# Kernel optimization log

Measured on AMD Instinct MI355X. Metric: run time of the kernel, lower is better.

Reference implementation:

```python
import jax, jax.numpy as jnp
import numpy as np


def setup_inputs() -> dict:
    key = jax.random.key(0)
    k0, k1, k2, k3 = jax.random.split(key, 4)
    B, T, C = 4, 2048, 1024
    x = jax.random.normal(k0, (B, T, C), dtype=jnp.float32)
    s = C ** -0.5  # init-scale for weights so activations stay O(1)
    Wq = jax.random.normal(k1, (C, C), dtype=jnp.float32) * s
    Wk = jax.random.normal(k2, (C, C), dtype=jnp.float32) * s
    Wv = jax.random.normal(k3, (C, C), dtype=jnp.float32) * s
    return {"x": x, "Wq": Wq, "Wk": Wk, "Wv": Wv}


def reference(x, Wq, Wk, Wv):
    B, T, C = x.shape
    # torch nn.Linear: y = x @ W.T
    q = jnp.einsum('btc,dc->btd', x, Wq)
    k = jnp.einsum('btc,dc->btd', x, Wk)
    v = jnp.einsum('btc,dc->btd', x, Wv)
    scale = C ** -0.5
    wei = jnp.einsum('btd,bsd->bts', q, k) * scale  # [B, T, T]
    causal = jnp.tril(jnp.ones((T, T), dtype=bool))
    wei = jnp.where(causal, wei, -jnp.inf)
    wei = jax.nn.softmax(wei, axis=-1)
    out = jnp.einsum('bts,bsd->btd', wei, v)
    return out
```

## Files before the change

### kernel.cpp

```cpp
#include <hip/hip_runtime.h>
#include <hip/hip_bf16.h>
#include <math.h>

#define B_ 4
#define T_ 2048
#define C_ 1024
#define M_ (B_*T_)

typedef __attribute__((ext_vector_type(8))) __bf16 bf16x8;
typedef __attribute__((ext_vector_type(4))) float floatx4;

__device__ inline float bf2f(unsigned short u){
    return __uint_as_float(((unsigned)u) << 16);
}
__device__ inline unsigned short f2bf(float f){
    unsigned u = __float_as_uint(f);
    unsigned r = (u + 0x7fffu + ((u >> 16) & 1u)) >> 16;
    return (unsigned short)r;
}

__device__ inline void llds16(const unsigned short* g, unsigned short* lds){
    __builtin_amdgcn_global_load_lds(
        (const __attribute__((address_space(1))) unsigned int*)g,
        (__attribute__((address_space(3))) unsigned int*)(unsigned int)(uintptr_t)lds,
        16, 0, 0);
}

#define NX_ (M_*C_/4)
#define NW_ (C_*C_/4)
#define NL4_ (M_/4)
__global__ __launch_bounds__(256) void cast_all(
    const float* __restrict__ x, const float* __restrict__ wq,
    const float* __restrict__ wk, const float* __restrict__ wv,
    unsigned short* __restrict__ xb, unsigned short* __restrict__ wb,
    float* __restrict__ l)
{
    int i = blockIdx.x * 256 + threadIdx.x;
    const float* src; unsigned short* dst; int idx;
    if (i < NX_){ src = x; dst = xb; idx = i; }
    else if (i < NX_ + 3 * NW_){
        i -= NX_;
        int w = i / NW_; idx = i - w * NW_;
        src = (w == 0) ? wq : ((w == 1) ? wk : wv);
        dst = wb + (size_t)w * C_ * C_;
    } else {
        ((float4*)l)[i - NX_ - 3 * NW_] = make_float4(0.f, 0.f, 0.f, 0.f);
        return;
    }
    float4 v = ((const float4*)src)[idx];
    ((ushort4*)dst)[idx] = make_ushort4(f2bf(v.x), f2bf(v.y), f2bf(v.z), f2bf(v.w));
}

template<int WM, int WN>
__device__ inline void gemm_core(const unsigned short* __restrict__ A,
                                 const unsigned short* __restrict__ Bm,
                                 int lda, int ldb, int m0, int n0, int kTiles,
                                 unsigned short* As, unsigned short* Bs,
                                 floatx4 (*acc)[WN/16])
{
    const int tid  = threadIdx.x;
    const int lane = tid & 63;
    const int wave = tid >> 6;
    const int wm = (wave >> 1) * WM;
    const int wn = (wave & 1) * WN;
    const int fr = lane & 15;
    const int fq = lane >> 4;
    const int cxor = fr & 7;
    const int sr = lane >> 3;
    const int sc = ((lane & 7) ^ ((lane >> 3) & 7)) * 8;

    const unsigned short* gA = A  + (size_t)(m0 + wave * (WM/2) + sr) * lda + sc;
    const unsigned short* gB = Bm + (size_t)(n0 + wave * (WN/2) + sr) * ldb + sc;
    unsigned short* ldsA = As + wave * (WM/2) * 64;
    unsigned short* ldsB = Bs + wave * (WN/2) * 64;

    for (int kt = 0; kt < kTiles; kt++){
        const int k0 = kt * 64;
        __syncthreads();
        #pragma unroll
        for (int i = 0; i < WM/16; i++)
            llds16(gA + (size_t)(i * 8) * lda + k0, ldsA + i * 8 * 64);
        #pragma unroll
        for (int i = 0; i < WN/16; i++)
            llds16(gB + (size_t)(i * 8) * ldb + k0, ldsB + i * 8 * 64);
        __syncthreads();
        #pragma unroll
        for (int ks = 0; ks < 64; ks += 32){
            const int cpos = (((ks >> 3) + fq) ^ cxor) * 8;
            bf16x8 af[WM/16], bv[WN/16];
            #pragma unroll
            for (int i = 0; i < WM/16; i++)
                af[i] = *(const bf16x8*)(As + (wm + i*16 + fr) * 64 + cpos);
            #pragma unroll
            for (int j = 0; j < WN/16; j++)
                bv[j] = *(const bf16x8*)(Bs + (wn + j*16 + fr) * 64 + cpos);
            #pragma unroll
            for (int i = 0; i < WM/16; i++)
                #pragma unroll
                for (int j = 0; j < WN/16; j++)
                    acc[i][j] = __builtin_amdgcn_mfma_f32_16x16x32_bf16(af[i], bv[j], acc[i][j], 0, 0, 0);
        }
    }
}

template<int WM, int WN>
__device__ inline void gemm_core8(const unsigned short* __restrict__ A,
                                  const unsigned short* __restrict__ Bm,
                                  int lda, int ldb, int m0, int n0, int kTiles,
                                  unsigned short* As, unsigned short* Bs,
                                  floatx4 (*acc)[WN/16])
{
    const int tid  = threadIdx.x;
    const int lane = tid & 63;
    const int wave = tid >> 6;
    const int wm = (wave >> 1) * WM;
    const int wn = (wave & 1) * WN;
    const int fr = lane & 15;
    const int fq = lane >> 4;
    const int cxor = fr & 7;
    const int sr = lane >> 3;
    const int sc = ((lane & 7) ^ ((lane >> 3) & 7)) * 8;

    const unsigned short* gA = A  + (size_t)(m0 + wave * (WM/2) + sr) * lda + sc;
    const unsigned short* gB = Bm + (size_t)(n0 + wave * (WN/4) + sr) * ldb + sc;
    unsigned short* ldsA = As + wave * (WM/2) * 64;
    unsigned short* ldsB = Bs + wave * (WN/4) * 64;

    for (int kt = 0; kt < kTiles; kt++){
        const int k0 = kt * 64;
        __syncthreads();
        #pragma unroll
        for (int i = 0; i < WM/16; i++)
            llds16(gA + (size_t)(i * 8) * lda + k0, ldsA + i * 8 * 64);
        #pragma unroll
        for (int i = 0; i < WN/32; i++)
            llds16(gB + (size_t)(i * 8) * ldb + k0, ldsB + i * 8 * 64);
        __syncthreads();
        #pragma unroll
        for (int ks = 0; ks < 64; ks += 32){
            const int cpos = (((ks >> 3) + fq) ^ cxor) * 8;
            bf16x8 af[WM/16], bv[WN/16];
            #pragma unroll
            for (int i = 0; i < WM/16; i++)
                af[i] = *(const bf16x8*)(As + (wm + i*16 + fr) * 64 + cpos);
            #pragma unroll
            for (int j = 0; j < WN/16; j++)
                bv[j] = *(const bf16x8*)(Bs + (wn + j*16 + fr) * 64 + cpos);
            #pragma unroll
            for (int i = 0; i < WM/16; i++)
                #pragma unroll
                for (int j = 0; j < WN/16; j++)
                    acc[i][j] = __builtin_amdgcn_mfma_f32_16x16x32_bf16(af[i], bv[j], acc[i][j], 0, 0, 0);
        }
    }
}

__global__ __launch_bounds__(256, 4) void proj_gemm(
    const unsigned short* __restrict__ xb,
    const unsigned short* __restrict__ Wb,
    unsigned short* __restrict__ Qb, unsigned short* __restrict__ Kb,
    unsigned short* __restrict__ Vt)
{
    __shared__ unsigned short As[128 * 64];
    __shared__ unsigned short Bs[128 * 64];
    const int L = blockIdx.x;
    const int k = L & 7, j = L >> 3;
    const int m0 = (k * 8 + (j & 7)) * 128;
    const int n0 = ((j >> 3) & 7) * 128;
    const int z  = j >> 6;
    const unsigned short* W = Wb + (size_t)z * C_ * C_;

    floatx4 acc[4][4];
    #pragma unroll
    for (int i = 0; i < 4; i++)
        #pragma unroll
        for (int jj = 0; jj < 4; jj++) acc[i][jj] = (floatx4){0.f,0.f,0.f,0.f};
    gemm_core<64, 64>(xb, W, C_, C_, m0, n0, C_ / 64, As, Bs, acc);

    const int lane = threadIdx.x & 63, wave = threadIdx.x >> 6;
    const int wm = (wave >> 1) * 64, wn = (wave & 1) * 64;
    const int fr = lane & 15, fq = lane >> 4;

    if (z < 2){
        unsigned short* Y = z ? Kb : Qb;
        #pragma unroll
        for (int i = 0; i < 4; i++)
            #pragma unroll
            for (int jj = 0; jj < 4; jj++)
                #pragma unroll
                for (int r = 0; r < 4; r++){
                    int row = m0 + wm + i*16 + fq*4 + r;
                    int col = n0 + wn + jj*16 + fr;
                    Y[(size_t)row * C_ + col] = f2bf(acc[i][jj][r]);
                }
    } else {
        #pragma unroll
        for (int i = 0; i < 4; i++)
            #pragma unroll
            for (int jj = 0; jj < 4; jj++){
                int row = m0 + wm + i*16 + fq*4;
                int col = n0 + wn + jj*16 + fr;
                int b = row / T_, t = row % T_;
                ushort4 o = make_ushort4(f2bf(acc[i][jj][0]), f2bf(acc[i][jj][1]),
                                         f2bf(acc[i][jj][2]), f2bf(acc[i][jj][3]));
                *(ushort4*)&Vt[(size_t)b * C_ * T_ + (size_t)col * T_ + t] = o;
            }
    }
}

__global__ __launch_bounds__(512, 4) void score_gemm(
    const unsigned short* __restrict__ Qb, const unsigned short* __restrict__ Kb,
    unsigned short* __restrict__ P, float* __restrict__ l)
{
    const int L = blockIdx.x;
    const int xcd = L & 7, j = L >> 3;
    const int b  = xcd >> 1;
    const int p  = j / 17, rr = j % 17;
    const int kk = 2 * p + (xcd & 1);
    int ti, si;
    if (rr <= 15 - kk){ ti = 15 - kk; si = rr; }
    else              { ti = kk;      si = rr - (16 - kk); }
    const int t0 = ti * 128, s0 = si * 128;

    __shared__ unsigned short As[128 * 64];
    __shared__ unsigned short Bs[128 * 64];
    floatx4 acc[2][4];
    #pragma unroll
    for (int i = 0; i < 2; i++)
        #pragma unroll
        for (int jj = 0; jj < 4; jj++) acc[i][jj] = (floatx4){0.f,0.f,0.f,0.f};
    gemm_core8<32, 64>(Qb + (size_t)b * T_ * C_, Kb + (size_t)b * T_ * C_,
                       C_, C_, t0, s0, C_ / 64, As, Bs, acc);

    const int lane = threadIdx.x & 63, wave = threadIdx.x >> 6;
    const int wm = (wave >> 1) * 32, wn = (wave & 1) * 64;
    const int fr = lane & 15, fq = lane >> 4;
    unsigned short* Pb = P + (size_t)b * T_ * T_;
    const float scale = 0.03125f;
    float rsl[2][4];
    #pragma unroll
    for (int i = 0; i < 2; i++)
        #pragma unroll
        for (int r2 = 0; r2 < 4; r2++) rsl[i][r2] = 0.f;

    #pragma unroll
    for (int i = 0; i < 2; i++)
        #pragma unroll
        for (int jj = 0; jj < 4; jj++)
            #pragma unroll
            for (int r2 = 0; r2 < 4; r2++){
                int t = t0 + wm + i*16 + fq*4 + r2;
                int s = s0 + wn + jj*16 + fr;
                float v = (s <= t) ? __expf(acc[i][jj][r2] * scale) : 0.f;
                rsl[i][r2] += v;
                Pb[(size_t)t * T_ + s] = f2bf(v);
            }
    #pragma unroll
    for (int i = 0; i < 2; i++)
        #pragma unroll
        for (int r2 = 0; r2 < 4; r2++){
            float v = rsl[i][r2];
            v += __shfl_xor(v, 1, 64);
            v += __shfl_xor(v, 2, 64);
            v += __shfl_xor(v, 4, 64);
            v += __shfl_xor(v, 8, 64);
            if (fr == 0){
                int t = t0 + wm + i*16 + fq*4 + r2;
                atomicAdd(&l[(size_t)b * T_ + t], v);
            }
        }
}

__global__ __launch_bounds__(256, 4) void pv_gemm(
    const unsigned short* __restrict__ P, const unsigned short* __restrict__ Vt,
    const float* __restrict__ l, float* __restrict__ out)
{
    const int L = blockIdx.x;
    const int xcd = L & 7, j = L >> 3;
    const int b  = xcd >> 1;
    const int p  = j >> 4;
    const int n0 = (j & 15) * 64;
    const int kk = 2 * p + (xcd & 1);

    __shared__ unsigned short As[128 * 64];
    __shared__ unsigned short Bs[64 * 64];

    const int lane = threadIdx.x & 63, wave = threadIdx.x >> 6;
    const int wm = (wave >> 1) * 64, wn = (wave & 1) * 32;
    const int fr = lane & 15, fq = lane >> 4;
    float* ob = out + (size_t)b * T_ * C_;
    const float* lb = l + (size_t)b * T_;

    #pragma unroll
    for (int phase = 0; phase < 2; phase++){
        const int ti = phase ? kk : (15 - kk);
        const int t0 = ti * 128;
        const int kTiles = 2 * (ti + 1);

        floatx4 acc[4][2];
        #pragma unroll
        for (int i = 0; i < 4; i++)
            #pragma unroll
            for (int jj = 0; jj < 2; jj++) acc[i][jj] = (floatx4){0.f,0.f,0.f,0.f};
        gemm_core<64, 32>(P + (size_t)b * T_ * T_, Vt + (size_t)b * C_ * T_,
                          T_, T_, t0, n0, kTiles, As, Bs, acc);

        #pragma unroll
        for (int i = 0; i < 4; i++){
            float inv[4];
            #pragma unroll
            for (int r2 = 0; r2 < 4; r2++)
                inv[r2] = 1.f / lb[t0 + wm + i*16 + fq*4 + r2];
            #pragma unroll
            for (int jj = 0; jj < 2; jj++)
                #pragma unroll
                for (int r2 = 0; r2 < 4; r2++){
                    int t = t0 + wm + i*16 + fq*4 + r2;
                    int d = n0 + wn + jj*16 + fr;
                    ob[(size_t)t * C_ + d] = acc[i][jj][r2] * inv[r2];
                }
        }
    }
}

extern "C" void kernel_launch(void* const* d_in, const int* in_sizes, int n_in,
                              void* d_out, int out_size, void* d_ws, size_t ws_size,
                              hipStream_t stream)
{
    const float* x  = (const float*)d_in[0];
    const float* Wq = (const float*)d_in[1];
    const float* Wk = (const float*)d_in[2];
    const float* Wv = (const float*)d_in[3];
    float* out = (float*)d_out;

    unsigned short* Qb = (unsigned short*)d_ws;
    unsigned short* Kb = Qb + (size_t)M_ * C_;
    unsigned short* Vt = Kb + (size_t)M_ * C_;
    unsigned short* P  = Vt + (size_t)M_ * C_;
    float* l = (float*)(P + (size_t)M_ * T_);
    unsigned short* xb = P;
    unsigned short* Wb = P + (size_t)M_ * C_;

    cast_all<<<(NX_ + 3 * NW_ + NL4_ + 255) / 256, 256, 0, stream>>>(
        x, Wq, Wk, Wv, xb, Wb, l);
    proj_gemm <<<1536, 256, 0, stream>>>(xb, Wb, Qb, Kb, Vt);
    score_gemm<<<544, 512, 0, stream>>>(Qb, Kb, P, l);
    pv_gemm   <<<512, 256, 0, stream>>>(P, Vt, l, out);
}
```

Measured before the change: 203.4 us.

## Double-buffer LDS tiles with vmcnt-counted prefetch in score and PV GEMMs

Replaces the single-buffer load/sync/compute loop in the score and PV GEMM cores with double-buffered LDS. The next k-tile is issued via global_load_lds before the current one is computed, and explicit s_waitcnt vmcnt and barriers control the hazards. This is meant to hide global load latency behind MFMA work. It doubles LDS use per block, which may lower occupancy, and relies on hand-written waitcnt counts matching the issued loads.

```diff
diff --git a/kernel.cpp b/kernel.cpp
--- a/kernel.cpp
+++ b/kernel.cpp
@@ -25,6 +25,15 @@
         (__attribute__((address_space(3))) unsigned int*)(unsigned int)(uintptr_t)lds,
         16, 0, 0);
 }
+
+template<int N> __device__ inline void vmwait(){
+    static_assert(N==0 || N==4 || N==6 || N==8, "add literal");
+    if constexpr (N==0) asm volatile("s_waitcnt vmcnt(0)" ::: "memory");
+    else if constexpr (N==4) asm volatile("s_waitcnt vmcnt(4)" ::: "memory");
+    else if constexpr (N==6) asm volatile("s_waitcnt vmcnt(6)" ::: "memory");
+    else if constexpr (N==8) asm volatile("s_waitcnt vmcnt(8)" ::: "memory");
+}
+__device__ inline void lgkm0(){ asm volatile("s_waitcnt lgkmcnt(0)" ::: "memory"); }
 
 #define NX_ (M_*C_/4)
 #define NW_ (C_*C_/4)
@@ -104,12 +113,16 @@
 }
 
 template<int WM, int WN>
-__device__ inline void gemm_core8(const unsigned short* __restrict__ A,
-                                  const unsigned short* __restrict__ Bm,
-                                  int lda, int ldb, int m0, int n0, int kTiles,
-                                  unsigned short* As, unsigned short* Bs,
-                                  floatx4 (*acc)[WN/16])
-{
+__device__ inline void gemm_core_cnt(const unsigned short* __restrict__ A,
+                                     const unsigned short* __restrict__ Bm,
+                                     int lda, int ldb, int m0, int n0, int kTiles,
+                                     unsigned short* As, unsigned short* Bs,
+                                     floatx4 (*acc)[WN/16])
+{
+    const int NL  = WM/16 + WN/16;
+    const int ASZ = 2 * WM * 64;
+    const int BSZ = 2 * WN * 64;
+
     const int tid  = threadIdx.x;
     const int lane = tid & 63;
     const int wave = tid >> 6;
@@ -122,36 +135,132 @@
     const int sc = ((lane & 7) ^ ((lane >> 3) & 7)) * 8;
 
     const unsigned short* gA = A  + (size_t)(m0 + wave * (WM/2) + sr) * lda + sc;
+    const unsigned short* gB = Bm + (size_t)(n0 + wave * (WN/2) + sr) * ldb + sc;
+    unsigned short* ldsA = As + wave * (WM/2) * 64;
+    unsigned short* ldsB = Bs + wave * (WN/2) * 64;
+
+    __syncthreads();
+    #pragma unroll
+    for (int i = 0; i < WM/16; i++)
+        llds16(gA + (size_t)(i * 8) * lda, ldsA + i * 8 * 64);
+    #pragma unroll
+    for (int i = 0; i < WN/16; i++)
+        llds16(gB + (size_t)(i * 8) * ldb, ldsB + i * 8 * 64);
+
+    int cur = 0;
+    for (int kt = 0; kt < kTiles; kt++){
+        if (kt + 1 < kTiles){
+            const int nk0 = (kt + 1) * 64;
+            unsigned short* lA = ldsA + (cur ^ 1) * ASZ;
+            unsigned short* lB = ldsB + (cur ^ 1) * BSZ;
+            #pragma unroll
+            for (int i = 0; i < WM/16; i++)
+                llds16(gA + (size_t)(i * 8) * lda + nk0, lA + i * 8 * 64);
+            #pragma unroll
+            for (int i = 0; i < WN/16; i++)
+                llds16(gB + (size_t)(i * 8) * ldb + nk0, lB + i * 8 * 64);
+            vmwait<NL>();
+        } else {
+            vmwait<0>();
+        }
+        __builtin_amdgcn_s_barrier();
+        const unsigned short* rA = As + cur * ASZ;
+        const unsigned short* rB = Bs + cur * BSZ;
+        #pragma unroll
+        for (int ks = 0; ks < 64; ks += 32){
+            const int cpos = (((ks >> 3) + fq) ^ cxor) * 8;
+            bf16x8 af[WM/16], bv[WN/16];
+            #pragma unroll
+            for (int i = 0; i < WM/16; i++)
+                af[i] = *(const bf16x8*)(rA + (wm + i*16 + fr) * 64 + cpos);
+            #pragma unroll
+            for (int j = 0; j < WN/16; j++)
+                bv[j] = *(const bf16x8*)(rB + (wn + j*16 + fr) * 64 + cpos);
+            #pragma unroll
+            for (int i = 0; i < WM/16; i++)
+                #pragma unroll
+                for (int j = 0; j < WN/16; j++)
+                    acc[i][j] = __builtin_amdgcn_mfma_f32_16x16x32_bf16(af[i], bv[j], acc[i][j], 0, 0, 0);
+        }
+        lgkm0();
+        __builtin_amdgcn_s_barrier();
+        cur ^= 1;
+    }
+}
+
+template<int WM, int WN>
+__device__ inline void gemm_core8_cnt(const unsigned short* __restrict__ A,
+                                      const unsigned short* __restrict__ Bm,
+                                      int lda, int ldb, int m0, int n0, int kTiles,
+                                      unsigned short* As, unsigned short* Bs,
+                                      floatx4 (*acc)[WN/16])
+{
+    const int NL  = WM/16 + WN/32;
+    const int ASZ = 4 * WM * 64;
+    const int BSZ = 2 * WN * 64;
+
+    const int tid  = threadIdx.x;
+    const int lane = tid & 63;
+    const int wave = tid >> 6;
+    const int wm = (wave >> 1) * WM;
+    const int wn = (wave & 1) * WN;
+    const int fr = lane & 15;
+    const int fq = lane >> 4;
+    const int cxor = fr & 7;
+    const int sr = lane >> 3;
+    const int sc = ((lane & 7) ^ ((lane >> 3) & 7)) * 8;
+
+    const unsigned short* gA = A  + (size_t)(m0 + wave * (WM/2) + sr) * lda + sc;
     const unsigned short* gB = Bm + (size_t)(n0 + wave * (WN/4) + sr) * ldb + sc;
     unsigned short* ldsA = As + wave * (WM/2) * 64;
     unsigned short* ldsB = Bs + wave * (WN/4) * 64;
 
+    __syncthreads();
+    #pragma unroll
+    for (int i = 0; i < WM/16; i++)
+        llds16(gA + (size_t)(i * 8) * lda, ldsA + i * 8 * 64);
+    #pragma unroll
+    for (int i = 0; i < WN/32; i++)
+        llds16(gB + (size_t)(i * 8) * ldb, ldsB + i * 8 * 64);
+
+    int cur = 0;
     for (int kt = 0; kt < kTiles; kt++){
-        const int k0 = kt * 64;
-        __syncthreads();
-        #pragma unroll
-        for (int i = 0; i < WM/16; i++)
-            llds16(gA + (size_t)(i * 8) * lda + k0, ldsA + i * 8 * 64);
-        #pragma unroll
-        for (int i = 0; i < WN/32; i++)
-            llds16(gB + (size_t)(i * 8) * ldb + k0, ldsB + i * 8 * 64);
-        __syncthreads();
+        if (kt + 1 < kTiles){
+            const int nk0 = (kt + 1) * 64;
+            unsigned short* lA = ldsA + (cur ^ 1) * ASZ;
+            unsigned short* lB = ldsB + (cur ^ 1) * BSZ;
+            #pragma unroll
+            for (int i = 0; i < WM/16; i++)
+                llds16(gA + (size_t)(i * 8) * lda + nk0, lA + i * 8 * 64);
+            #pragma unroll
+            for (int i = 0; i < WN/32; i++)
+                llds16(gB + (size_t)(i * 8) * ldb + nk0, lB + i * 8 * 64);
+            vmwait<NL>();
+        } else {
+            vmwait<0>();
+        }
+        __builtin_amdgcn_s_barrier();
+        const unsigned short* rA = As + cur * ASZ;
+        const unsigned short* rB = Bs + cur * BSZ;
         #pragma unroll
         for (int ks = 0; ks < 64; ks += 32){
             const int cpos = (((ks >> 3) + fq) ^ cxor) * 8;
             bf16x8 af[WM/16], bv[WN/16];
             #pragma unroll
             for (int i = 0; i < WM/16; i++)
-                af[i] = *(const bf16x8*)(As + (wm + i*16 + fr) * 64 + cpos);
+                af[i] = *(const bf16x8*)(rA + (wm + i*16 + fr) * 64 + cpos);
             #pragma unroll
             for (int j = 0; j < WN/16; j++)
-                bv[j] = *(const bf16x8*)(Bs + (wn + j*16 + fr) * 64 + cpos);
+                bv[j] = *(const bf16x8*)(rB + (wn + j*16 + fr) * 64 + cpos);
             #pragma unroll
             for (int i = 0; i < WM/16; i++)
                 #pragma unroll
                 for (int j = 0; j < WN/16; j++)
                     acc[i][j] = __builtin_amdgcn_mfma_f32_16x16x32_bf16(af[i], bv[j], acc[i][j], 0, 0, 0);
         }
+        lgkm0();
+        __builtin_amdgcn_s_barrier();
+        cur ^= 1;
     }
 }
 
@@ -222,15 +331,15 @@
     else              { ti = kk;      si = rr - (16 - kk); }
     const int t0 = ti * 128, s0 = si * 128;
 
-    __shared__ unsigned short As[128 * 64];
-    __shared__ unsigned short Bs[128 * 64];
+    __shared__ unsigned short As[2 * 128 * 64];
+    __shared__ unsigned short Bs[2 * 128 * 64];
     floatx4 acc[2][4];
     #pragma unroll
     for (int i = 0; i < 2; i++)
         #pragma unroll
         for (int jj = 0; jj < 4; jj++) acc[i][jj] = (floatx4){0.f,0.f,0.f,0.f};
-    gemm_core8<32, 64>(Qb + (size_t)b * T_ * C_, Kb + (size_t)b * T_ * C_,
-                       C_, C_, t0, s0, C_ / 64, As, Bs, acc);
+    gemm_core8_cnt<32, 64>(Qb + (size_t)b * T_ * C_, Kb + (size_t)b * T_ * C_,
+                           C_, C_, t0, s0, C_ / 64, As, Bs, acc);
 
     const int lane = threadIdx.x & 63, wave = threadIdx.x >> 6;
     const int wm = (wave >> 1) * 32, wn = (wave & 1) * 64;
@@ -282,8 +391,8 @@
     const int n0 = (j & 15) * 64;
     const int kk = 2 * p + (xcd & 1);
 
-    __shared__ unsigned short As[128 * 64];
-    __shared__ unsigned short Bs[64 * 64];
+    __shared__ unsigned short As[2 * 128 * 64];
+    __shared__ unsigned short Bs[2 * 64 * 64];
 
     const int lane = threadIdx.x & 63, wave = threadIdx.x >> 6;
     const int wm = (wave >> 1) * 64, wn = (wave & 1) * 32;
@@ -302,8 +411,8 @@
         for (int i = 0; i < 4; i++)
             #pragma unroll
             for (int jj = 0; jj < 2; jj++) acc[i][jj] = (floatx4){0.f,0.f,0.f,0.f};
-        gemm_core<64, 32>(P + (size_t)b * T_ * T_, Vt + (size_t)b * C_ * T_,
-                          T_, T_, t0, n0, kTiles, As, Bs, acc);
+        gemm_core_cnt<64, 32>(P + (size_t)b * T_ * T_, Vt + (size_t)b * C_ * T_,
+                              T_, T_, t0, n0, kTiles, As, Bs, acc);
 
         #pragma unroll
         for (int i = 0; i < 4; i++){
```

Result: faster. 195.2 us (median of 2 runs) (-4.1%).
